# Performance work log

Hardware: AMD Instinct MI355X
Metric: run time of the kernel (lower is better)

Reference implementation:

```python
import jax, jax.numpy as jnp
import numpy as np
from jax import lax

LMBDA = 10.0
MAX_ITERATIONS = 100
MAX_DISTANCE = 5.0
B_, M_, N_ = 8, 1024, 1024


def sinkhorn(M, lmbda=LMBDA, max_iterations=MAX_ITERATIONS, max_distance=MAX_DISTANCE):
    # K = exp(-lmbda * clamp_max(M, max_distance)); uniform marginals r=1/m, c=1/n
    b, m, n = M.shape
    K = jnp.exp(-lmbda * jnp.minimum(M, max_distance))          # (b, m, n)
    KT = jnp.swapaxes(K, -2, -1)                                # (b, n, m)
    r = jnp.full((b, m, 1), 1.0 / m, dtype=M.dtype)
    c = jnp.full((b, n, 1), 1.0 / n, dtype=M.dtype)
    # Fixed-count Sinkhorn iterations (original breaks early on convergence;
    # running the full count reaches the same fixed point).
    def body(u, _):
        u = r / (K @ (c / (KT @ u)))
        return u, None
    u, _ = lax.scan(body, r, None, length=max_iterations)
    v = c / (KT @ u)                                            # (b, n, 1)
    P = u * K * jnp.swapaxes(v, -2, -1)                         # (b, m, n)
    return P


def setup_inputs() -> dict:
    key = jax.random.key(0)
    M = jax.random.uniform(key, (B_, M_, N_), dtype=jnp.float32)  # non-negative costs
    return {"M": M}


def reference(M):
    return sinkhorn(M)
```

## Files before the change

### kernel.cpp

```cpp
#include <hip/hip_runtime.h>
#include <math.h>


#define B_    8
#define N_    1024
#define G_    32
#define RPB   32
#define KSTR  1028
#define NITER 100
#define TPB   256
#define LMB   10.0f
#define MAXD  5.0f

#define LDS_FLOATS (RPB * KSTR + N_ + RPB + 4 * G_)

typedef unsigned long long u64;

__device__ __forceinline__ void st8(float* p, float a, float b) {
    float2 f2 = make_float2(a, b);
    __hip_atomic_store((u64*)p, __builtin_bit_cast(u64, f2),
                       __ATOMIC_RELAXED, __HIP_MEMORY_SCOPE_AGENT);
}
__device__ __forceinline__ float2 ld8(const float* p) {
    u64 raw = __hip_atomic_load((const u64*)p,
                                __ATOMIC_RELAXED, __HIP_MEMORY_SCOPE_AGENT);
    return __builtin_bit_cast(float2, raw);
}
__device__ __forceinline__ void publish(int* s, int v) {
    __atomic_signal_fence(__ATOMIC_SEQ_CST);
    __hip_atomic_store(s, v, __ATOMIC_RELAXED, __HIP_MEMORY_SCOPE_AGENT);
}
__device__ __forceinline__ void poll32(const int* st, int tgt) {
    const int l = threadIdx.x & 31;
    for (;;) {
        int s = __hip_atomic_load(&st[l], __ATOMIC_RELAXED,
                                  __HIP_MEMORY_SCOPE_AGENT);
        if (__all(s >= tgt)) break;
        __builtin_amdgcn_s_sleep(2);
    }
    __atomic_signal_fence(__ATOMIC_SEQ_CST);
}

__global__ void __launch_bounds__(TPB, 1)
sinkhorn_kernel(const float* __restrict__ Mg,
                float* __restrict__ Pg,
                float* __restrict__ part,
                float* __restrict__ vbuf,
                int* __restrict__ stA,
                int* __restrict__ stV)
{
    extern __shared__ float lds[];
    float* Kl   = lds;
    float* vl   = lds + RPB * KSTR;
    float* ul   = vl + N_;
    float4* red = (float4*)(ul + RPB);

    const int b    = blockIdx.x & (B_ - 1);
    const int g    = blockIdx.x >> 3;
    const int t    = threadIdx.x;
    const int row0 = g * RPB;
    const float r = 1.0f / (float)N_;
    const float c = 1.0f / (float)N_;

    const float* Mb = Mg + ((size_t)b * N_ + row0) * N_;
    for (int i = 0; i < RPB; ++i) {
        float4 m4 = ((const float4*)(Mb + (size_t)i * N_))[t];
        float4 k4;
        k4.x = expf(-LMB * fminf(m4.x, MAXD));
        k4.y = expf(-LMB * fminf(m4.y, MAXD));
        k4.z = expf(-LMB * fminf(m4.z, MAXD));
        k4.w = expf(-LMB * fminf(m4.w, MAXD));
        *(float4*)&Kl[i * KSTR + 4 * t] = k4;
    }
    if (t < RPB) ul[t] = r;
    __syncthreads();

    for (int it = 0; it <= NITER; ++it) {
        const int p   = it & 1;
        const int tgt = it + 1;
        int* stA_pb = stA + ((size_t)p * B_ + b) * G_;
        int* stV_pb = stV + ((size_t)p * B_ + b) * G_;

        float4 a = make_float4(0.f, 0.f, 0.f, 0.f);
#pragma unroll
        for (int i = 0; i < RPB; ++i) {
            const float u  = ul[i];
            const float4 k4 = *(const float4*)&Kl[i * KSTR + 4 * t];
            a.x = fmaf(k4.x, u, a.x);
            a.y = fmaf(k4.y, u, a.y);
            a.z = fmaf(k4.z, u, a.z);
            a.w = fmaf(k4.w, u, a.w);
        }
        float* slot = part + (((size_t)p * B_ + b) * G_ + g) * N_;
        st8(&slot[4 * t],     a.x, a.y);
        st8(&slot[4 * t + 2], a.z, a.w);

        __syncthreads();
        if (t == 0) publish(&stA_pb[g], tgt);

        poll32(stA_pb, tgt);
        {
            const int gp = t >> 3;
            const int q  = t & 7;
            const float* pb = part + (((size_t)p * B_ + b) * G_ + gp) * N_
                            + 32 * g + 4 * q;
            float2 s0 = ld8(pb);
            float2 s1 = ld8(pb + 2);
            float4 acc = make_float4(s0.x, s0.y, s1.x, s1.y);
#pragma unroll
            for (int d = 8; d <= 32; d <<= 1) {
                acc.x += __shfl_xor(acc.x, d);
                acc.y += __shfl_xor(acc.y, d);
                acc.z += __shfl_xor(acc.z, d);
                acc.w += __shfl_xor(acc.w, d);
            }
            const int wv = t >> 6;
            if ((t & 63) < 8) red[wv * 8 + (t & 63)] = acc;
        }
        __syncthreads();
        float* vb = vbuf + ((size_t)p * B_ + b) * N_;
        if (t < 8) {
            float4 y4;
            y4.x = red[t].x + red[8 + t].x + red[16 + t].x + red[24 + t].x;
            y4.y = red[t].y + red[8 + t].y + red[16 + t].y + red[24 + t].y;
            y4.z = red[t].z + red[8 + t].z + red[16 + t].z + red[24 + t].z;
            y4.w = red[t].w + red[8 + t].w + red[16 + t].w + red[24 + t].w;
            st8(&vb[32 * g + 4 * t],     c / y4.x, c / y4.y);
            st8(&vb[32 * g + 4 * t + 2], c / y4.z, c / y4.w);
        }
        if (t == 0) {
            __atomic_signal_fence(__ATOMIC_SEQ_CST);
            __builtin_amdgcn_s_waitcnt(0);
            publish(&stV_pb[g], tgt);
        }

        poll32(stV_pb, tgt);
        {
            float2 w0 = ld8(&vb[4 * t]);
            float2 w1 = ld8(&vb[4 * t + 2]);
            *(float4*)&vl[4 * t] = make_float4(w0.x, w0.y, w1.x, w1.y);
        }
        __syncthreads();

        if (it == NITER) break;

        const int rI = t >> 3;
        const int l  = t & 7;
        float4 za = make_float4(0.f, 0.f, 0.f, 0.f);
#pragma unroll
        for (int k2 = 0; k2 < 32; ++k2) {
            const int j0 = 4 * l + 32 * k2;
            const float4 k4 = *(const float4*)&Kl[rI * KSTR + j0];
            const float4 vv = *(const float4*)&vl[j0];
            za.x = fmaf(k4.x, vv.x, za.x);
            za.y = fmaf(k4.y, vv.y, za.y);
            za.z = fmaf(k4.z, vv.z, za.z);
            za.w = fmaf(k4.w, vv.w, za.w);
        }
        float z = za.x + za.y + za.z + za.w;
        z += __shfl_xor(z, 1);
        z += __shfl_xor(z, 2);
        z += __shfl_xor(z, 4);
        if (l == 0) ul[rI] = r / z;
        __syncthreads();
    }

    float* Pb = Pg + ((size_t)b * N_ + row0) * N_;
    const float4 v4 = *(const float4*)&vl[4 * t];
    for (int i = 0; i < RPB; ++i) {
        const float u  = ul[i];
        const float4 k4 = *(const float4*)&Kl[i * KSTR + 4 * t];
        float4 p4;
        p4.x = u * k4.x * v4.x;
        p4.y = u * k4.y * v4.y;
        p4.z = u * k4.z * v4.z;
        p4.w = u * k4.w * v4.w;
        ((float4*)(Pb + (size_t)i * N_))[t] = p4;
    }
}

extern "C" void kernel_launch(void* const* d_in, const int* in_sizes, int n_in,
                              void* d_out, int out_size, void* d_ws, size_t ws_size,
                              hipStream_t stream) {
    const float* M = (const float*)d_in[0];
    float* P = (float*)d_out;

    const size_t part_floats = (size_t)2 * B_ * G_ * N_;
    const size_t v_floats    = (size_t)2 * B_ * N_;
    float* part = (float*)d_ws;
    float* vbuf = part + part_floats;
    int*   stA  = (int*)(vbuf + v_floats);
    int*   stV  = stA + 2 * B_ * G_;
    hipMemsetAsync(stA, 0, (size_t)4 * B_ * G_ * sizeof(int), stream);

    const size_t lds_bytes = (size_t)LDS_FLOATS * sizeof(float);
    (void)hipFuncSetAttribute((const void*)sinkhorn_kernel,
                              hipFuncAttributeMaxDynamicSharedMemorySize,
                              (int)lds_bytes);

    void* args[] = { (void*)&M, (void*)&P, (void*)&part, (void*)&vbuf,
                     (void*)&stA, (void*)&stV };
    hipError_t e = hipLaunchCooperativeKernel((void*)sinkhorn_kernel,
                                              dim3(B_ * G_), dim3(TPB),
                                              args, (unsigned)lds_bytes, stream);
    if (e != hipSuccess) {
        sinkhorn_kernel<<<dim3(B_ * G_), dim3(TPB), lds_bytes, stream>>>(
            M, P, part, vbuf, stA, stV);
    }
}
```

Before: 618.1 us.

## Replace flag-based cross-block sync with iteration-stamped packed value words

Each partial sum and each v entry is now stored as a 64-bit word that holds the float and the iteration number. Readers spin until every word they need carries the current iteration stamp. This removes the separate status arrays, the block barrier and publish before each poll, and the double buffering by parity. The goal is to cut the per-iteration latency of the two grid-wide handoffs. In exchange, global traffic for partials and v doubles, there are more polled loads, and the workspace memset grows to cover all the packed buffers.

```diff
diff --git a/kernel.cpp b/kernel.cpp
--- a/kernel.cpp
+++ b/kernel.cpp
@@ -15,39 +15,28 @@
 #define LDS_FLOATS (RPB * KSTR + N_ + RPB + 4 * G_)
 
 typedef unsigned long long u64;
-
-__device__ __forceinline__ void st8(float* p, float a, float b) {
-    float2 f2 = make_float2(a, b);
-    __hip_atomic_store((u64*)p, __builtin_bit_cast(u64, f2),
-                       __ATOMIC_RELAXED, __HIP_MEMORY_SCOPE_AGENT);
-}
-__device__ __forceinline__ float2 ld8(const float* p) {
-    u64 raw = __hip_atomic_load((const u64*)p,
-                                __ATOMIC_RELAXED, __HIP_MEMORY_SCOPE_AGENT);
-    return __builtin_bit_cast(float2, raw);
-}
-__device__ __forceinline__ void publish(int* s, int v) {
-    __atomic_signal_fence(__ATOMIC_SEQ_CST);
-    __hip_atomic_store(s, v, __ATOMIC_RELAXED, __HIP_MEMORY_SCOPE_AGENT);
-}
-__device__ __forceinline__ void poll32(const int* st, int tgt) {
-    const int l = threadIdx.x & 31;
-    for (;;) {
-        int s = __hip_atomic_load(&st[l], __ATOMIC_RELAXED,
-                                  __HIP_MEMORY_SCOPE_AGENT);
-        if (__all(s >= tgt)) break;
-        __builtin_amdgcn_s_sleep(2);
-    }
-    __atomic_signal_fence(__ATOMIC_SEQ_CST);
+typedef unsigned int u32;
+
+__device__ __forceinline__ u64 pack(float v, u32 s) {
+    return (u64)__float_as_uint(v) | ((u64)s << 32);
+}
+__device__ __forceinline__ float pval(u64 w) {
+    return __uint_as_float((u32)w);
+}
+__device__ __forceinline__ u32 pst(u64 w) { return (u32)(w >> 32); }
+
+__device__ __forceinline__ void ast(u64* p, u64 v) {
+    __hip_atomic_store(p, v, __ATOMIC_RELAXED, __HIP_MEMORY_SCOPE_AGENT);
+}
+__device__ __forceinline__ u64 ald(const u64* p) {
+    return __hip_atomic_load(p, __ATOMIC_RELAXED, __HIP_MEMORY_SCOPE_AGENT);
 }
 
 __global__ void __launch_bounds__(TPB, 1)
 sinkhorn_kernel(const float* __restrict__ Mg,
                 float* __restrict__ Pg,
-                float* __restrict__ part,
-                float* __restrict__ vbuf,
-                int* __restrict__ stA,
-                int* __restrict__ stV)
+                u64* __restrict__ ppk,
+                u64* __restrict__ vpk)
 {
     extern __shared__ float lds[];
     float* Kl   = lds;
@@ -75,11 +64,11 @@
     if (t < RPB) ul[t] = r;
     __syncthreads();
 
+    u64* ppk_b = ppk + (size_t)b * G_ * N_;
+    u64* vpk_b = vpk + (size_t)b * N_;
+
     for (int it = 0; it <= NITER; ++it) {
-        const int p   = it & 1;
-        const int tgt = it + 1;
-        int* stA_pb = stA + ((size_t)p * B_ + b) * G_;
-        int* stV_pb = stV + ((size_t)p * B_ + b) * G_;
+        const u32 st = (u32)(it + 1);
 
         float4 a = make_float4(0.f, 0.f, 0.f, 0.f);
 #pragma unroll
@@ -91,22 +80,27 @@
             a.z = fmaf(k4.z, u, a.z);
             a.w = fmaf(k4.w, u, a.w);
         }
-        float* slot = part + (((size_t)p * B_ + b) * G_ + g) * N_;
-        st8(&slot[4 * t],     a.x, a.y);
-        st8(&slot[4 * t + 2], a.z, a.w);
-
-        __syncthreads();
-        if (t == 0) publish(&stA_pb[g], tgt);
-
-        poll32(stA_pb, tgt);
+        {
+            u64* slot = ppk_b + (size_t)g * N_ + 4 * t;
+            ast(slot + 0, pack(a.x, st));
+            ast(slot + 1, pack(a.y, st));
+            ast(slot + 2, pack(a.z, st));
+            ast(slot + 3, pack(a.w, st));
+        }
+
         {
             const int gp = t >> 3;
             const int q  = t & 7;
-            const float* pb = part + (((size_t)p * B_ + b) * G_ + gp) * N_
-                            + 32 * g + 4 * q;
-            float2 s0 = ld8(pb);
-            float2 s1 = ld8(pb + 2);
-            float4 acc = make_float4(s0.x, s0.y, s1.x, s1.y);
+            const u64* src = ppk_b + (size_t)gp * N_ + 32 * g + 4 * q;
+            u64 w0, w1, w2, w3;
+            for (;;) {
+                w0 = ald(src + 0); w1 = ald(src + 1);
+                w2 = ald(src + 2); w3 = ald(src + 3);
+                if ((pst(w0) == st) & (pst(w1) == st) &
+                    (pst(w2) == st) & (pst(w3) == st)) break;
+                __builtin_amdgcn_s_sleep(1);
+            }
+            float4 acc = make_float4(pval(w0), pval(w1), pval(w2), pval(w3));
 #pragma unroll
             for (int d = 8; d <= 32; d <<= 1) {
                 acc.x += __shfl_xor(acc.x, d);
@@ -114,31 +108,34 @@
                 acc.z += __shfl_xor(acc.z, d);
                 acc.w += __shfl_xor(acc.w, d);
             }
-            const int wv = t >> 6;
-            if ((t & 63) < 8) red[wv * 8 + (t & 63)] = acc;
+            if ((t & 63) < 8) red[(t >> 6) * 8 + (t & 63)] = acc;
         }
         __syncthreads();
-        float* vb = vbuf + ((size_t)p * B_ + b) * N_;
         if (t < 8) {
             float4 y4;
             y4.x = red[t].x + red[8 + t].x + red[16 + t].x + red[24 + t].x;
             y4.y = red[t].y + red[8 + t].y + red[16 + t].y + red[24 + t].y;
             y4.z = red[t].z + red[8 + t].z + red[16 + t].z + red[24 + t].z;
             y4.w = red[t].w + red[8 + t].w + red[16 + t].w + red[24 + t].w;
-            st8(&vb[32 * g + 4 * t],     c / y4.x, c / y4.y);
-            st8(&vb[32 * g + 4 * t + 2], c / y4.z, c / y4.w);
-        }
-        if (t == 0) {
-            __atomic_signal_fence(__ATOMIC_SEQ_CST);
-            __builtin_amdgcn_s_waitcnt(0);
-            publish(&stV_pb[g], tgt);
-        }
-
-        poll32(stV_pb, tgt);
+            u64* vdst = vpk_b + 32 * g + 4 * t;
+            ast(vdst + 0, pack(c / y4.x, st));
+            ast(vdst + 1, pack(c / y4.y, st));
+            ast(vdst + 2, pack(c / y4.z, st));
+            ast(vdst + 3, pack(c / y4.w, st));
+        }
+
         {
-            float2 w0 = ld8(&vb[4 * t]);
-            float2 w1 = ld8(&vb[4 * t + 2]);
-            *(float4*)&vl[4 * t] = make_float4(w0.x, w0.y, w1.x, w1.y);
+            const u64* vsrc = vpk_b + 4 * t;
+            u64 w0, w1, w2, w3;
+            for (;;) {
+                w0 = ald(vsrc + 0); w1 = ald(vsrc + 1);
+                w2 = ald(vsrc + 2); w3 = ald(vsrc + 3);
+                if ((pst(w0) == st) & (pst(w1) == st) &
+                    (pst(w2) == st) & (pst(w3) == st)) break;
+                __builtin_amdgcn_s_sleep(1);
+            }
+            *(float4*)&vl[4 * t] =
+                make_float4(pval(w0), pval(w1), pval(w2), pval(w3));
         }
         __syncthreads();
 
@@ -185,26 +182,23 @@
     const float* M = (const float*)d_in[0];
     float* P = (float*)d_out;
 
-    const size_t part_floats = (size_t)2 * B_ * G_ * N_;
-    const size_t v_floats    = (size_t)2 * B_ * N_;
-    float* part = (float*)d_ws;
-    float* vbuf = part + part_floats;
-    int*   stA  = (int*)(vbuf + v_floats);
-    int*   stV  = stA + 2 * B_ * G_;
-    hipMemsetAsync(stA, 0, (size_t)4 * B_ * G_ * sizeof(int), stream);
+    u64* ppk = (u64*)d_ws;
+    u64* vpk = ppk + (size_t)B_ * G_ * N_;
+    hipMemsetAsync(d_ws, 0,
+                   ((size_t)B_ * G_ * N_ + (size_t)B_ * N_) * sizeof(u64),
+                   stream);
 
     const size_t lds_bytes = (size_t)LDS_FLOATS * sizeof(float);
     (void)hipFuncSetAttribute((const void*)sinkhorn_kernel,
                               hipFuncAttributeMaxDynamicSharedMemorySize,
                               (int)lds_bytes);
 
-    void* args[] = { (void*)&M, (void*)&P, (void*)&part, (void*)&vbuf,
-                     (void*)&stA, (void*)&stV };
+    void* args[] = { (void*)&M, (void*)&P, (void*)&ppk, (void*)&vpk };
     hipError_t e = hipLaunchCooperativeKernel((void*)sinkhorn_kernel,
                                               dim3(B_ * G_), dim3(TPB),
                                               args, (unsigned)lds_bytes, stream);
     if (e != hipSuccess) {
         sinkhorn_kernel<<<dim3(B_ * G_), dim3(TPB), lds_bytes, stream>>>(
-            M, P, part, vbuf, stA, stV);
-    }
-}
+            M, P, ppk, vpk);
+    }
+}
```

Result: slower. 1.413 ms (+128.7%).

## Cache the K tile in registers for both matvec phases

Applied to the files above, without the earlier changes.

Each thread preloads its K slices into registers: 32 float4 for the column-sum phase and 32 float4 for the row-sum phase, so the loop no longer reads K from LDS on every iteration. The row-sum phase is remapped so each thread handles 4 rows by 32 columns, and u is read as vectorised float4 loads. This removes LDS bandwidth and latency from the per-iteration critical path. In exchange it uses about 256 extra VGPRs per thread, which risks spills even with launch bounds of one block.

```diff
diff --git a/kernel.cpp b/kernel.cpp
--- a/kernel.cpp
+++ b/kernel.cpp
@@ -59,6 +59,8 @@
     const int g    = blockIdx.x >> 3;
     const int t    = threadIdx.x;
     const int row0 = g * RPB;
+    const int rq   = t >> 5;
+    const int cq   = t & 31;
     const float r = 1.0f / (float)N_;
     const float c = 1.0f / (float)N_;
 
@@ -75,21 +77,42 @@
     if (t < RPB) ul[t] = r;
     __syncthreads();
 
+    float4 ka[RPB];
+#pragma unroll
+    for (int i = 0; i < RPB; ++i)
+        ka[i] = *(const float4*)&Kl[i * KSTR + 4 * t];
+    float4 kb[4][8];
+#pragma unroll
+    for (int ri = 0; ri < 4; ++ri)
+#pragma unroll
+        for (int jj = 0; jj < 8; ++jj)
+            kb[ri][jj] = *(const float4*)&Kl[(4 * rq + ri) * KSTR
+                                             + 4 * cq + 128 * jj];
+    __syncthreads();
+
     for (int it = 0; it <= NITER; ++it) {
         const int p   = it & 1;
         const int tgt = it + 1;
         int* stA_pb = stA + ((size_t)p * B_ + b) * G_;
         int* stV_pb = stV + ((size_t)p * B_ + b) * G_;
 
+        float4 uu[8];
+#pragma unroll
+        for (int q = 0; q < 8; ++q)
+            uu[q] = *(const float4*)&ul[4 * q];
         float4 a = make_float4(0.f, 0.f, 0.f, 0.f);
 #pragma unroll
-        for (int i = 0; i < RPB; ++i) {
-            const float u  = ul[i];
-            const float4 k4 = *(const float4*)&Kl[i * KSTR + 4 * t];
-            a.x = fmaf(k4.x, u, a.x);
-            a.y = fmaf(k4.y, u, a.y);
-            a.z = fmaf(k4.z, u, a.z);
-            a.w = fmaf(k4.w, u, a.w);
+        for (int q = 0; q < 8; ++q) {
+            const float us[4] = { uu[q].x, uu[q].y, uu[q].z, uu[q].w };
+#pragma unroll
+            for (int e = 0; e < 4; ++e) {
+                const float4 k4 = ka[4 * q + e];
+                const float u = us[e];
+                a.x = fmaf(k4.x, u, a.x);
+                a.y = fmaf(k4.y, u, a.y);
+                a.z = fmaf(k4.z, u, a.z);
+                a.w = fmaf(k4.w, u, a.w);
+            }
         }
         float* slot = part + (((size_t)p * B_ + b) * G_ + g) * N_;
         st8(&slot[4 * t],     a.x, a.y);
@@ -114,8 +137,7 @@
                 acc.z += __shfl_xor(acc.z, d);
                 acc.w += __shfl_xor(acc.w, d);
             }
-            const int wv = t >> 6;
-            if ((t & 63) < 8) red[wv * 8 + (t & 63)] = acc;
+            if ((t & 63) < 8) red[(t >> 6) * 8 + (t & 63)] = acc;
         }
         __syncthreads();
         float* vb = vbuf + ((size_t)p * B_ + b) * N_;
@@ -144,24 +166,32 @@
 
         if (it == NITER) break;
 
-        const int rI = t >> 3;
-        const int l  = t & 7;
-        float4 za = make_float4(0.f, 0.f, 0.f, 0.f);
-#pragma unroll
-        for (int k2 = 0; k2 < 32; ++k2) {
-            const int j0 = 4 * l + 32 * k2;
-            const float4 k4 = *(const float4*)&Kl[rI * KSTR + j0];
-            const float4 vv = *(const float4*)&vl[j0];
-            za.x = fmaf(k4.x, vv.x, za.x);
-            za.y = fmaf(k4.y, vv.y, za.y);
-            za.z = fmaf(k4.z, vv.z, za.z);
-            za.w = fmaf(k4.w, vv.w, za.w);
-        }
-        float z = za.x + za.y + za.z + za.w;
-        z += __shfl_xor(z, 1);
-        z += __shfl_xor(z, 2);
-        z += __shfl_xor(z, 4);
-        if (l == 0) ul[rI] = r / z;
+        float z0 = 0.f, z1 = 0.f, z2 = 0.f, z3 = 0.f;
+#pragma unroll
+        for (int jj = 0; jj < 8; ++jj) {
+            const float4 vv = *(const float4*)&vl[4 * cq + 128 * jj];
+            z0 = fmaf(kb[0][jj].x, vv.x, z0); z0 = fmaf(kb[0][jj].y, vv.y, z0);
+            z0 = fmaf(kb[0][jj].z, vv.z, z0); z0 = fmaf(kb[0][jj].w, vv.w, z0);
+            z1 = fmaf(kb[1][jj].x, vv.x, z1); z1 = fmaf(kb[1][jj].y, vv.y, z1);
+            z1 = fmaf(kb[1][jj].z, vv.z, z1); z1 = fmaf(kb[1][jj].w, vv.w, z1);
+            z2 = fmaf(kb[2][jj].x, vv.x, z2); z2 = fmaf(kb[2][jj].y, vv.y, z2);
+            z2 = fmaf(kb[2][jj].z, vv.z, z2); z2 = fmaf(kb[2][jj].w, vv.w, z2);
+            z3 = fmaf(kb[3][jj].x, vv.x, z3); z3 = fmaf(kb[3][jj].y, vv.y, z3);
+            z3 = fmaf(kb[3][jj].z, vv.z, z3); z3 = fmaf(kb[3][jj].w, vv.w, z3);
+        }
+#pragma unroll
+        for (int d = 1; d <= 16; d <<= 1) {
+            z0 += __shfl_xor(z0, d);
+            z1 += __shfl_xor(z1, d);
+            z2 += __shfl_xor(z2, d);
+            z3 += __shfl_xor(z3, d);
+        }
+        if (cq == 0) {
+            ul[4 * rq + 0] = r / z0;
+            ul[4 * rq + 1] = r / z1;
+            ul[4 * rq + 2] = r / z2;
+            ul[4 * rq + 3] = r / z3;
+        }
         __syncthreads();
     }
 
@@ -169,7 +199,7 @@
     const float4 v4 = *(const float4*)&vl[4 * t];
     for (int i = 0; i < RPB; ++i) {
         const float u  = ul[i];
-        const float4 k4 = *(const float4*)&Kl[i * KSTR + 4 * t];
+        const float4 k4 = ka[i];
         float4 p4;
         p4.x = u * k4.x * v4.x;
         p4.y = u * k4.y * v4.y;
```

Result: slower. 661.7 us (+7.1%).

## Pair two batches per block to interleave their cross-block sync phases

Applied to the files above, without the earlier changes.

Each block now owns 16 rows from each of two batch elements instead of 32 rows from one. The two batches' reduce and broadcast steps are interleaved so that polling for one batch's flags overlaps compute for the other, aiming to hide inter-block synchronisation latency. The parity double-buffering of partials and v is dropped, relying on the flag ordering to prevent overwrites, and the poll sleep is shortened. The cost is that each batch is now split across 64 groups, so every sync polls twice as many flags and the column reduction has more partials to combine.

```diff
diff --git a/kernel.cpp b/kernel.cpp
--- a/kernel.cpp
+++ b/kernel.cpp
@@ -4,15 +4,16 @@
 
 #define B_    8
 #define N_    1024
-#define G_    32
-#define RPB   32
+#define NP    4
+#define G2    64
+#define RPB2  16
 #define KSTR  1028
 #define NITER 100
 #define TPB   256
 #define LMB   10.0f
 #define MAXD  5.0f
 
-#define LDS_FLOATS (RPB * KSTR + N_ + RPB + 4 * G_)
+#define LDS_FLOATS (2 * RPB2 * KSTR + 2 * N_ + 2 * RPB2 + 4 * 32)
 
 typedef unsigned long long u64;
 
@@ -30,13 +31,13 @@
     __atomic_signal_fence(__ATOMIC_SEQ_CST);
     __hip_atomic_store(s, v, __ATOMIC_RELAXED, __HIP_MEMORY_SCOPE_AGENT);
 }
-__device__ __forceinline__ void poll32(const int* st, int tgt) {
-    const int l = threadIdx.x & 31;
+__device__ __forceinline__ void poll64(const int* st, int tgt) {
+    const int l = threadIdx.x & 63;
     for (;;) {
         int s = __hip_atomic_load(&st[l], __ATOMIC_RELAXED,
                                   __HIP_MEMORY_SCOPE_AGENT);
         if (__all(s >= tgt)) break;
-        __builtin_amdgcn_s_sleep(2);
+        __builtin_amdgcn_s_sleep(1);
     }
     __atomic_signal_fence(__ATOMIC_SEQ_CST);
 }
@@ -50,132 +51,196 @@
                 int* __restrict__ stV)
 {
     extern __shared__ float lds[];
-    float* Kl   = lds;
-    float* vl   = lds + RPB * KSTR;
-    float* ul   = vl + N_;
-    float4* red = (float4*)(ul + RPB);
-
-    const int b    = blockIdx.x & (B_ - 1);
-    const int g    = blockIdx.x >> 3;
+    float* KX   = lds;
+    float* KY   = KX + RPB2 * KSTR;
+    float* vlX  = KY + RPB2 * KSTR;
+    float* vlY  = vlX + N_;
+    float* ulX  = vlY + N_;
+    float* ulY  = ulX + RPB2;
+    float4* redX = (float4*)(ulY + RPB2);
+    float4* redY = redX + 16;
+
+    const int pr   = blockIdx.x & (NP - 1);
+    const int g    = blockIdx.x >> 2;
+    const int bx   = 2 * pr;
+    const int by   = 2 * pr + 1;
     const int t    = threadIdx.x;
-    const int row0 = g * RPB;
+    const int row0 = g * RPB2;
     const float r = 1.0f / (float)N_;
     const float c = 1.0f / (float)N_;
 
-    const float* Mb = Mg + ((size_t)b * N_ + row0) * N_;
-    for (int i = 0; i < RPB; ++i) {
-        float4 m4 = ((const float4*)(Mb + (size_t)i * N_))[t];
-        float4 k4;
-        k4.x = expf(-LMB * fminf(m4.x, MAXD));
-        k4.y = expf(-LMB * fminf(m4.y, MAXD));
-        k4.z = expf(-LMB * fminf(m4.z, MAXD));
-        k4.w = expf(-LMB * fminf(m4.w, MAXD));
-        *(float4*)&Kl[i * KSTR + 4 * t] = k4;
-    }
-    if (t < RPB) ul[t] = r;
+    const float* MbX = Mg + ((size_t)bx * N_ + row0) * N_;
+    const float* MbY = Mg + ((size_t)by * N_ + row0) * N_;
+    for (int i = 0; i < RPB2; ++i) {
+        float4 mx = ((const float4*)(MbX + (size_t)i * N_))[t];
+        float4 my = ((const float4*)(MbY + (size_t)i * N_))[t];
+        float4 kx, ky;
+        kx.x = expf(-LMB * fminf(mx.x, MAXD));
+        kx.y = expf(-LMB * fminf(mx.y, MAXD));
+        kx.z = expf(-LMB * fminf(mx.z, MAXD));
+        kx.w = expf(-LMB * fminf(mx.w, MAXD));
+        ky.x = expf(-LMB * fminf(my.x, MAXD));
+        ky.y = expf(-LMB * fminf(my.y, MAXD));
+        ky.z = expf(-LMB * fminf(my.z, MAXD));
+        ky.w = expf(-LMB * fminf(my.w, MAXD));
+        *(float4*)&KX[i * KSTR + 4 * t] = kx;
+        *(float4*)&KY[i * KSTR + 4 * t] = ky;
+    }
+    if (t < RPB2) { ulX[t] = r; ulY[t] = r; }
     __syncthreads();
 
+    int* stA_x = stA + bx * G2;
+    int* stA_y = stA + by * G2;
+    int* stV_x = stV + bx * G2;
+    int* stV_y = stV + by * G2;
+    float* pxs = part + (size_t)(bx * G2 + g) * N_;
+    float* pys = part + (size_t)(by * G2 + g) * N_;
+    float* vbX = vbuf + (size_t)bx * N_;
+    float* vbY = vbuf + (size_t)by * N_;
+
     for (int it = 0; it <= NITER; ++it) {
-        const int p   = it & 1;
         const int tgt = it + 1;
-        int* stA_pb = stA + ((size_t)p * B_ + b) * G_;
-        int* stV_pb = stV + ((size_t)p * B_ + b) * G_;
-
-        float4 a = make_float4(0.f, 0.f, 0.f, 0.f);
-#pragma unroll
-        for (int i = 0; i < RPB; ++i) {
-            const float u  = ul[i];
-            const float4 k4 = *(const float4*)&Kl[i * KSTR + 4 * t];
-            a.x = fmaf(k4.x, u, a.x);
-            a.y = fmaf(k4.y, u, a.y);
-            a.z = fmaf(k4.z, u, a.z);
-            a.w = fmaf(k4.w, u, a.w);
-        }
-        float* slot = part + (((size_t)p * B_ + b) * G_ + g) * N_;
-        st8(&slot[4 * t],     a.x, a.y);
-        st8(&slot[4 * t + 2], a.z, a.w);
-
-        __syncthreads();
-        if (t == 0) publish(&stA_pb[g], tgt);
-
-        poll32(stA_pb, tgt);
-        {
-            const int gp = t >> 3;
-            const int q  = t & 7;
-            const float* pb = part + (((size_t)p * B_ + b) * G_ + gp) * N_
-                            + 32 * g + 4 * q;
-            float2 s0 = ld8(pb);
-            float2 s1 = ld8(pb + 2);
+
+        {
+            float4 aX = make_float4(0.f, 0.f, 0.f, 0.f);
+            float4 aY = make_float4(0.f, 0.f, 0.f, 0.f);
+#pragma unroll
+            for (int i = 0; i < RPB2; ++i) {
+                const float ux = ulX[i], uy = ulY[i];
+                const float4 kx = *(const float4*)&KX[i * KSTR + 4 * t];
+                const float4 ky = *(const float4*)&KY[i * KSTR + 4 * t];
+                aX.x = fmaf(kx.x, ux, aX.x); aX.y = fmaf(kx.y, ux, aX.y);
+                aX.z = fmaf(kx.z, ux, aX.z); aX.w = fmaf(kx.w, ux, aX.w);
+                aY.x = fmaf(ky.x, uy, aY.x); aY.y = fmaf(ky.y, uy, aY.y);
+                aY.z = fmaf(ky.z, uy, aY.z); aY.w = fmaf(ky.w, uy, aY.w);
+            }
+            st8(&pxs[4 * t],     aX.x, aX.y);
+            st8(&pxs[4 * t + 2], aX.z, aX.w);
+            st8(&pys[4 * t],     aY.x, aY.y);
+            st8(&pys[4 * t + 2], aY.z, aY.w);
+        }
+        __syncthreads();
+        if (t == 0) { publish(&stA_x[g], tgt); publish(&stA_y[g], tgt); }
+
+        poll64(stA_x, tgt);
+        {
+            const int gp = t >> 2, q = t & 3;
+            const float* pb = part + (size_t)(bx * G2 + gp) * N_
+                            + 16 * g + 4 * q;
+            float2 s0 = ld8(pb), s1 = ld8(pb + 2);
             float4 acc = make_float4(s0.x, s0.y, s1.x, s1.y);
 #pragma unroll
-            for (int d = 8; d <= 32; d <<= 1) {
+            for (int d = 4; d <= 32; d <<= 1) {
                 acc.x += __shfl_xor(acc.x, d);
                 acc.y += __shfl_xor(acc.y, d);
                 acc.z += __shfl_xor(acc.z, d);
                 acc.w += __shfl_xor(acc.w, d);
             }
-            const int wv = t >> 6;
-            if ((t & 63) < 8) red[wv * 8 + (t & 63)] = acc;
-        }
-        __syncthreads();
-        float* vb = vbuf + ((size_t)p * B_ + b) * N_;
-        if (t < 8) {
+            if ((t & 63) < 4) redX[(t >> 6) * 4 + (t & 63)] = acc;
+        }
+        poll64(stA_y, tgt);
+        {
+            const int gp = t >> 2, q = t & 3;
+            const float* pb = part + (size_t)(by * G2 + gp) * N_
+                            + 16 * g + 4 * q;
+            float2 s0 = ld8(pb), s1 = ld8(pb + 2);
+            float4 acc = make_float4(s0.x, s0.y, s1.x, s1.y);
+#pragma unroll
+            for (int d = 4; d <= 32; d <<= 1) {
+                acc.x += __shfl_xor(acc.x, d);
+                acc.y += __shfl_xor(acc.y, d);
+                acc.z += __shfl_xor(acc.z, d);
+                acc.w += __shfl_xor(acc.w, d);
+            }
+            if ((t & 63) < 4) redY[(t >> 6) * 4 + (t & 63)] = acc;
+        }
+        __syncthreads();
+        if (t < 4) {
             float4 y4;
-            y4.x = red[t].x + red[8 + t].x + red[16 + t].x + red[24 + t].x;
-            y4.y = red[t].y + red[8 + t].y + red[16 + t].y + red[24 + t].y;
-            y4.z = red[t].z + red[8 + t].z + red[16 + t].z + red[24 + t].z;
-            y4.w = red[t].w + red[8 + t].w + red[16 + t].w + red[24 + t].w;
-            st8(&vb[32 * g + 4 * t],     c / y4.x, c / y4.y);
-            st8(&vb[32 * g + 4 * t + 2], c / y4.z, c / y4.w);
+            y4.x = redX[t].x + redX[4 + t].x + redX[8 + t].x + redX[12 + t].x;
+            y4.y = redX[t].y + redX[4 + t].y + redX[8 + t].y + redX[12 + t].y;
+            y4.z = redX[t].z + redX[4 + t].z + redX[8 + t].z + redX[12 + t].z;
+            y4.w = redX[t].w + redX[4 + t].w + redX[8 + t].w + redX[12 + t].w;
+            st8(&vbX[16 * g + 4 * t],     c / y4.x, c / y4.y);
+            st8(&vbX[16 * g + 4 * t + 2], c / y4.z, c / y4.w);
+        } else if (t < 8) {
+            const int i = t - 4;
+            float4 y4;
+            y4.x = redY[i].x + redY[4 + i].x + redY[8 + i].x + redY[12 + i].x;
+            y4.y = redY[i].y + redY[4 + i].y + redY[8 + i].y + redY[12 + i].y;
+            y4.z = redY[i].z + redY[4 + i].z + redY[8 + i].z + redY[12 + i].z;
+            y4.w = redY[i].w + redY[4 + i].w + redY[8 + i].w + redY[12 + i].w;
+            st8(&vbY[16 * g + 4 * i],     c / y4.x, c / y4.y);
+            st8(&vbY[16 * g + 4 * i + 2], c / y4.z, c / y4.w);
         }
         if (t == 0) {
             __atomic_signal_fence(__ATOMIC_SEQ_CST);
             __builtin_amdgcn_s_waitcnt(0);
-            publish(&stV_pb[g], tgt);
-        }
-
-        poll32(stV_pb, tgt);
-        {
-            float2 w0 = ld8(&vb[4 * t]);
-            float2 w1 = ld8(&vb[4 * t + 2]);
-            *(float4*)&vl[4 * t] = make_float4(w0.x, w0.y, w1.x, w1.y);
-        }
-        __syncthreads();
-
+            publish(&stV_x[g], tgt); publish(&stV_y[g], tgt);
+        }
+
+        poll64(stV_x, tgt);
+        {
+            float2 w0 = ld8(&vbX[4 * t]), w1 = ld8(&vbX[4 * t + 2]);
+            *(float4*)&vlX[4 * t] = make_float4(w0.x, w0.y, w1.x, w1.y);
+        }
+        __syncthreads();
+        if (it < NITER) {
+            const int rI = t >> 4, l = t & 15;
+            float z = 0.f;
+#pragma unroll
+            for (int k = 0; k < 16; ++k) {
+                const int j0 = 4 * l + 64 * k;
+                const float4 kx = *(const float4*)&KX[rI * KSTR + j0];
+                const float4 vv = *(const float4*)&vlX[j0];
+                z = fmaf(kx.x, vv.x, z); z = fmaf(kx.y, vv.y, z);
+                z = fmaf(kx.z, vv.z, z); z = fmaf(kx.w, vv.w, z);
+            }
+            z += __shfl_xor(z, 1); z += __shfl_xor(z, 2);
+            z += __shfl_xor(z, 4); z += __shfl_xor(z, 8);
+            if (l == 0) ulX[rI] = r / z;
+        }
+
+        poll64(stV_y, tgt);
+        {
+            float2 w0 = ld8(&vbY[4 * t]), w1 = ld8(&vbY[4 * t + 2]);
+            *(float4*)&vlY[4 * t] = make_float4(w0.x, w0.y, w1.x, w1.y);
+        }
+        __syncthreads();
         if (it == NITER) break;
-
-        const int rI = t >> 3;
-        const int l  = t & 7;
-        float4 za = make_float4(0.f, 0.f, 0.f, 0.f);
-#pragma unroll
-        for (int k2 = 0; k2 < 32; ++k2) {
-            const int j0 = 4 * l + 32 * k2;
-            const float4 k4 = *(const float4*)&Kl[rI * KSTR + j0];
-            const float4 vv = *(const float4*)&vl[j0];
-            za.x = fmaf(k4.x, vv.x, za.x);
-            za.y = fmaf(k4.y, vv.y, za.y);
-            za.z = fmaf(k4.z, vv.z, za.z);
-            za.w = fmaf(k4.w, vv.w, za.w);
-        }
-        float z = za.x + za.y + za.z + za.w;
-        z += __shfl_xor(z, 1);
-        z += __shfl_xor(z, 2);
-        z += __shfl_xor(z, 4);
-        if (l == 0) ul[rI] = r / z;
-        __syncthreads();
-    }
-
-    float* Pb = Pg + ((size_t)b * N_ + row0) * N_;
-    const float4 v4 = *(const float4*)&vl[4 * t];
-    for (int i = 0; i < RPB; ++i) {
-        const float u  = ul[i];
-        const float4 k4 = *(const float4*)&Kl[i * KSTR + 4 * t];
-        float4 p4;
-        p4.x = u * k4.x * v4.x;
-        p4.y = u * k4.y * v4.y;
-        p4.z = u * k4.z * v4.z;
-        p4.w = u * k4.w * v4.w;
-        ((float4*)(Pb + (size_t)i * N_))[t] = p4;
+        {
+            const int rI = t >> 4, l = t & 15;
+            float z = 0.f;
+#pragma unroll
+            for (int k = 0; k < 16; ++k) {
+                const int j0 = 4 * l + 64 * k;
+                const float4 ky = *(const float4*)&KY[rI * KSTR + j0];
+                const float4 vv = *(const float4*)&vlY[j0];
+                z = fmaf(ky.x, vv.x, z); z = fmaf(ky.y, vv.y, z);
+                z = fmaf(ky.z, vv.z, z); z = fmaf(ky.w, vv.w, z);
+            }
+            z += __shfl_xor(z, 1); z += __shfl_xor(z, 2);
+            z += __shfl_xor(z, 4); z += __shfl_xor(z, 8);
+            if (l == 0) ulY[rI] = r / z;
+        }
+        __syncthreads();
+    }
+
+    float* PbX = Pg + ((size_t)bx * N_ + row0) * N_;
+    float* PbY = Pg + ((size_t)by * N_ + row0) * N_;
+    const float4 vx = *(const float4*)&vlX[4 * t];
+    const float4 vy = *(const float4*)&vlY[4 * t];
+    for (int i = 0; i < RPB2; ++i) {
+        const float ux = ulX[i], uy = ulY[i];
+        const float4 kx = *(const float4*)&KX[i * KSTR + 4 * t];
+        const float4 ky = *(const float4*)&KY[i * KSTR + 4 * t];
+        float4 px, py;
+        px.x = ux * kx.x * vx.x; px.y = ux * kx.y * vx.y;
+        px.z = ux * kx.z * vx.z; px.w = ux * kx.w * vx.w;
+        py.x = uy * ky.x * vy.x; py.y = uy * ky.y * vy.y;
+        py.z = uy * ky.z * vy.z; py.w = uy * ky.w * vy.w;
+        ((float4*)(PbX + (size_t)i * N_))[t] = px;
+        ((float4*)(PbY + (size_t)i * N_))[t] = py;
     }
 }
 
@@ -185,13 +250,13 @@
     const float* M = (const float*)d_in[0];
     float* P = (float*)d_out;
 
-    const size_t part_floats = (size_t)2 * B_ * G_ * N_;
-    const size_t v_floats    = (size_t)2 * B_ * N_;
+    const size_t part_floats = (size_t)B_ * G2 * N_;
+    const size_t v_floats    = (size_t)B_ * N_;
     float* part = (float*)d_ws;
     float* vbuf = part + part_floats;
     int*   stA  = (int*)(vbuf + v_floats);
-    int*   stV  = stA + 2 * B_ * G_;
-    hipMemsetAsync(stA, 0, (size_t)4 * B_ * G_ * sizeof(int), stream);
+    int*   stV  = stA + B_ * G2;
+    (void)hipMemsetAsync(stA, 0, (size_t)2 * B_ * G2 * sizeof(int), stream);
 
     const size_t lds_bytes = (size_t)LDS_FLOATS * sizeof(float);
     (void)hipFuncSetAttribute((const void*)sinkhorn_kernel,
@@ -201,10 +266,10 @@
     void* args[] = { (void*)&M, (void*)&P, (void*)&part, (void*)&vbuf,
                      (void*)&stA, (void*)&stV };
     hipError_t e = hipLaunchCooperativeKernel((void*)sinkhorn_kernel,
-                                              dim3(B_ * G_), dim3(TPB),
+                                              dim3(B_ * 32), dim3(TPB),
                                               args, (unsigned)lds_bytes, stream);
     if (e != hipSuccess) {
-        sinkhorn_kernel<<<dim3(B_ * G_), dim3(TPB), lds_bytes, stream>>>(
+        sinkhorn_kernel<<<dim3(B_ * 32), dim3(TPB), lds_bytes, stream>>>(
             M, P, part, vbuf, stA, stV);
     }
 }
```

New measurement: 1.417 ms. 129% more time.
